# Optimization experiments

Hardware: AMD Instinct MI355X
Metric: run time of the kernel (lower is better)

The kernel has to match this reference:

```python
import jax, jax.numpy as jnp
import numpy as np

N, E, B = 50000, 400000, 8
ND, ED, H, L = 32, 16, 128, 3

def setup_inputs() -> dict:
    key = jax.random.key(0)
    ks = jax.random.split(key, 32)
    s = 0.05
    inp = {
        'x': jax.random.normal(ks[0], (N, ND), jnp.float32),
        'edge_attr': jax.random.normal(ks[1], (E, ED), jnp.float32),
        'global_feature': jax.random.normal(ks[2], (B, 1), jnp.float32),
        'edge_index': jax.random.randint(ks[3], (2, E), 0, N, jnp.int64),
        'batch': jnp.sort(jax.random.randint(ks[4], (N,), 0, B, jnp.int64)),
        # embeddings
        'Wn': jax.random.normal(ks[5], (ND, H), jnp.float32) * s,
        'bn': jnp.zeros((H,), jnp.float32),
        'We': jax.random.normal(ks[6], (ED, H), jnp.float32) * s,
        'be': jnp.zeros((H,), jnp.float32),
        'Wg': jax.random.normal(ks[7], (1, H), jnp.float32) * s,
        'bg': jnp.zeros((H,), jnp.float32),
        # message-passing layers (stacked over L)
        'mW1': jax.random.normal(ks[8], (L, 3 * H, H), jnp.float32) * s,
        'mb1': jnp.zeros((L, H), jnp.float32),
        'mW2': jax.random.normal(ks[9], (L, H, H), jnp.float32) * s,
        'mb2': jnp.zeros((L, H), jnp.float32),
        'uW1': jax.random.normal(ks[10], (L, 2 * H, H), jnp.float32) * s,
        'ub1': jnp.zeros((L, H), jnp.float32),
        'uW2': jax.random.normal(ks[11], (L, H, H), jnp.float32) * s,
        'ub2': jnp.zeros((L, H), jnp.float32),
        # readout MLP
        'rW1': jax.random.normal(ks[12], (2 * H, H), jnp.float32) * s,
        'rb1': jnp.zeros((H,), jnp.float32),
        'rW2': jax.random.normal(ks[13], (H, H // 2), jnp.float32) * s,
        'rb2': jnp.zeros((H // 2,), jnp.float32),
        'rW3': jax.random.normal(ks[14], (H // 2, 1), jnp.float32) * s,
        'rb3': jnp.zeros((1,), jnp.float32),
    }
    return inp

def reference(x, edge_attr, global_feature, Wn, bn, We, be, Wg, bg,
              mW1, mb1, mW2, mb2, uW1, ub1, uW2, ub2,
              rW1, rb1, rW2, rb2, rW3, rb3, edge_index, batch):
    h = x @ Wn + bn                      # [N,H]
    e = edge_attr @ We + be              # [E,H]
    g = global_feature @ Wg + bg         # [B,H]
    src, dst = edge_index[0], edge_index[1]  # PyG: x_j=source, x_i=target, aggregate at target
    for l in range(L):
        m_in = jnp.concatenate([h[dst], h[src], e], axis=1)            # [E,3H]
        m = jax.nn.relu(m_in @ mW1[l] + mb1[l]) @ mW2[l] + mb2[l]       # [E,H]
        aggr = jax.ops.segment_sum(m, dst, num_segments=N)              # [N,H]
        u_in = jnp.concatenate([h, aggr], axis=1)                       # [N,2H]
        upd = jax.nn.relu(u_in @ uW1[l] + ub1[l]) @ uW2[l] + ub2[l]
        h = h + upd
    counts = jax.ops.segment_sum(jnp.ones((N,), h.dtype), batch, num_segments=B)
    pooled = jax.ops.segment_sum(h, batch, num_segments=B) / jnp.maximum(counts, 1.0)[:, None]
    final = jnp.concatenate([pooled, g], axis=1)                        # [B,2H]
    out = jax.nn.relu(final @ rW1 + rb1)
    out = jax.nn.relu(out @ rW2 + rb2)
    return out @ rW3 + rb3                                              # [B,1]
```

## Files before the change

### kernel.cpp

```cpp
#include <hip/hip_runtime.h>

#define NN 50000
#define NPAD 50048
#define NE 400000
#define NBATCH 8
#define NDIM 32
#define EDIM 16
#define H 128
#define NLAYERS 3
#define CHUNK_ELEMS 4096
#define NODE_CHUNKS 24
#define ZW_CHUNK 8192
#define NSB 196
#define ZEB 128

#define EMB_B 1563
#define DEG_B 1563
#define ZWB (NLAYERS * 8)
#define WEFB NLAYERS
#define WUB (NLAYERS * 257)
#define P1_B (EMB_B + DEG_B + ZWB + WEFB + WUB)
#define K2_B (NSB + NLAYERS + NLAYERS * NODE_CHUNKS)
#define ZDZS_B (NPAD / 64)
#define ZE_B (NE / ZEB)
#define ZZ_B (ZDZS_B + ZE_B)

typedef __attribute__((ext_vector_type(8))) __bf16 bf16x8;
typedef __attribute__((ext_vector_type(16))) float f32x16;
typedef __attribute__((ext_vector_type(8))) short short8;
typedef __attribute__((ext_vector_type(2))) float v2f;

__device__ __forceinline__ void block_sync_lds() {
  asm volatile("s_waitcnt lgkmcnt(0)\ns_barrier" ::: "memory");
}
__device__ __forceinline__ v2f bf2f(unsigned u) {
  v2f r;
  r.x = __uint_as_float(u << 16);
  r.y = __uint_as_float(u & 0xffff0000u);
  return r;
}

__global__ __launch_bounds__(256) void p1_kernel(
    const float* __restrict__ x, const float* __restrict__ Wn,
    const float* __restrict__ bn, __bf16* __restrict__ hb,
    const int* __restrict__ ei, int* __restrict__ deg,
    const float* __restrict__ mW1, __bf16* __restrict__ ZW,
    const float* __restrict__ mb1, const float* __restrict__ We,
    const float* __restrict__ be, float* __restrict__ Wef,
    float* __restrict__ bm, const float* __restrict__ uW1,
    const float* __restrict__ mW2, const float* __restrict__ mb2,
    float* __restrict__ Wu, float* __restrict__ va) {
  __shared__ __align__(16) float smem[NDIM * H + 32 * NDIM];
  int bi = blockIdx.x;
  int tid = threadIdx.x;
  if (bi < EMB_B) {
    float* Ws = smem;
    float* xs = smem + NDIM * H;
    int nbase = bi * 32;
    for (int f = tid; f < NDIM * H; f += 256) Ws[f] = Wn[f];
    for (int f = tid; f < 32 * NDIM; f += 256) {
      int gi = nbase * NDIM + f;
      xs[f] = (gi < NN * NDIM) ? x[gi] : 0.f;
    }
    __syncthreads();
    int j = tid & 127, g = tid >> 7;
    float b = bn[j];
    for (int nn = 0; nn < 16; ++nn) {
      int node = nbase + g * 16 + nn;
      if (node < NN) {
        float acc = b;
#pragma unroll
        for (int k = 0; k < NDIM; ++k)
          acc = fmaf(xs[(g * 16 + nn) * NDIM + k], Ws[k * H + j], acc);
        hb[(size_t)node * H + j] = (__bf16)acc;
      }
    }
  } else if (bi < EMB_B + DEG_B) {
    int e = (bi - EMB_B) * 256 + tid;
    if (e < NE) atomicAdd(&deg[ei[NE + e]], 1);
  } else if (bi < EMB_B + DEG_B + ZWB) {
    int bb = bi - EMB_B - DEG_B;
    int l = bb / 8;
    int c = bb % 8;
    const float* w1 = mW1 + (size_t)l * 384 * H;
    __bf16* dst = ZW + ((size_t)l * 8 + c) * ZW_CHUNK;
    for (int it = 0; it < 32; it += 4) {
      float wv[4];
#pragma unroll
      for (int q = 0; q < 4; ++q) {
        int flat = (it + q) * 256 + tid;
        int j = flat & 7;
        int lane = (flat >> 3) & 63;
        int nt = (flat >> 9) & 7;
        int k = c * 16 + ((lane >> 5) << 3) + j;
        int n = nt * 32 + (lane & 31);
        wv[q] = (n < 128) ? w1[(size_t)k * H + n]
                          : w1[(size_t)(128 + k) * H + (n - 128)];
      }
#pragma unroll
      for (int q = 0; q < 4; ++q) {
        int flat = (it + q) * 256 + tid;
        int hilo = flat >> 12;
        __bf16 hi = (__bf16)wv[q];
        __bf16 lo = (__bf16)(wv[q] - (float)hi);
        dst[flat] = hilo ? lo : hi;
      }
    }
  } else if (bi < EMB_B + DEG_B + ZWB + WEFB) {
    int l = bi - (EMB_B + DEG_B + ZWB);
    float* WeS = smem;
    float* beS = smem + 2048;
    for (int f = tid; f < EDIM * H; f += 256) WeS[f] = We[f];
    if (tid < 128) beS[tid] = be[tid];
    __syncthreads();
    if (tid < 128) {
      int n = tid;
      const float* w1 = mW1 + (size_t)l * 384 * H + (size_t)256 * H + n;
      float acc[EDIM];
#pragma unroll
      for (int i = 0; i < EDIM; ++i) acc[i] = 0.f;
      float accb = 0.f;
      for (int c = 0; c < H; c += 4) {
        float w0 = w1[(size_t)(c + 0) * H];
        float w1v = w1[(size_t)(c + 1) * H];
        float w2 = w1[(size_t)(c + 2) * H];
        float w3 = w1[(size_t)(c + 3) * H];
        accb = fmaf(beS[c + 0], w0, accb);
        accb = fmaf(beS[c + 1], w1v, accb);
        accb = fmaf(beS[c + 2], w2, accb);
        accb = fmaf(beS[c + 3], w3, accb);
#pragma unroll
        for (int i = 0; i < EDIM; ++i) {
          acc[i] = fmaf(WeS[i * H + c + 0], w0, acc[i]);
          acc[i] = fmaf(WeS[i * H + c + 1], w1v, acc[i]);
          acc[i] = fmaf(WeS[i * H + c + 2], w2, acc[i]);
          acc[i] = fmaf(WeS[i * H + c + 3], w3, acc[i]);
        }
      }
#pragma unroll
      for (int i = 0; i < EDIM; ++i)
        Wef[((size_t)l * EDIM + i) * H + n] = acc[i];
      bm[l * H + n] = mb1[l * H + n] + accb;
    }
  } else {
    int bb = bi - (EMB_B + DEG_B + ZWB + WEFB);
    int l = bb / 257;
    int r = bb % 257;
    int j = tid & 127, hf = tid >> 7;
    const float* u1 = uW1 + (size_t)l * 256 * H;
    if (r < 128) {
      if (tid < 128) Wu[((size_t)l * 256 + r) * H + j] = u1[(size_t)r * H + j];
    } else {
      float* rowS = smem;
      float* redS = smem + 128;
      if (tid < 128)
        rowS[tid] = (r < 256) ? mW2[((size_t)l * H + (r - 128)) * H + tid]
                              : mb2[l * H + tid];
      __syncthreads();
      int cb = hf * 64;
      float s0 = 0.f, s1 = 0.f, s2 = 0.f, s3 = 0.f;
      for (int c = 0; c < 64; c += 4) {
        float a0 = u1[(size_t)(128 + cb + c + 0) * H + j];
        float a1 = u1[(size_t)(128 + cb + c + 1) * H + j];
        float a2 = u1[(size_t)(128 + cb + c + 2) * H + j];
        float a3 = u1[(size_t)(128 + cb + c + 3) * H + j];
        s0 = fmaf(rowS[cb + c + 0], a0, s0);
        s1 = fmaf(rowS[cb + c + 1], a1, s1);
        s2 = fmaf(rowS[cb + c + 2], a2, s2);
        s3 = fmaf(rowS[cb + c + 3], a3, s3);
      }
      float s = (s0 + s1) + (s2 + s3);
      if (hf == 1) redS[j] = s;
      __syncthreads();
      if (hf == 0) {
        float tot = s + redS[j];
        if (r < 256) Wu[((size_t)l * 256 + r) * H + j] = tot;
        else va[l * H + j] = tot;
      }
    }
  }
}

__global__ __launch_bounds__(256) void k2_kernel(
    const int* __restrict__ deg, int* __restrict__ bsum,
    const float* __restrict__ Wef, __bf16* __restrict__ WefS,
    const float* __restrict__ Wu, const float* __restrict__ uW2,
    __bf16* __restrict__ WnS) {
  __shared__ int ws[4];
  int bi = blockIdx.x;
  int tid = threadIdx.x;
  if (bi < NSB) {
    int i = bi * 256 + tid;
    int lane = tid & 63, wid = tid >> 6;
    int v = (i < NN) ? deg[i] : 0;
#pragma unroll
    for (int off = 32; off; off >>= 1) v += __shfl_down(v, off);
    if (lane == 0) ws[wid] = v;
    __syncthreads();
    if (tid == 0) bsum[bi] = ws[0] + ws[1] + ws[2] + ws[3];
  } else if (bi < NSB + NLAYERS) {
    int l = bi - NSB;
    int nt = tid >> 6, lane = tid & 63;
    int n = nt * 32 + (lane & 31);
    int half = lane >> 5;
    const float* wl = Wef + (size_t)l * EDIM * H;
    __bf16* dst = WefS + (size_t)l * CHUNK_ELEMS;
#pragma unroll
    for (int j = 0; j < 8; ++j) {
      int k = half * 8 + j;
      float w = wl[(size_t)k * H + n];
      __bf16 hi = (__bf16)w;
      __bf16 lo = (__bf16)(w - (float)hi);
      dst[((0 * 4 + nt) * 64 + lane) * 8 + j] = hi;
      dst[((1 * 4 + nt) * 64 + lane) * 8 + j] = lo;
    }
  } else {
    int idx = bi - NSB - NLAYERS;
    int l = idx / NODE_CHUNKS;
    int c = idx % NODE_CHUNKS;
    int nt = tid >> 6, lane = tid & 63;
    int n = nt * 32 + (lane & 31);
    int half = lane >> 5;
    __bf16* dst = WnS + ((size_t)l * NODE_CHUNKS + c) * CHUNK_ELEMS;
#pragma unroll
    for (int j = 0; j < 8; ++j) {
      float w;
      if (c < 16) {
        int k = c * 16 + half * 8 + j;
        w = Wu[((size_t)l * 256 + k) * H + n];
      } else {
        int k = (c - 16) * 16 + half * 8 + j;
        w = uW2[((size_t)l * H + k) * H + n];
      }
      __bf16 hi = (__bf16)w;
      __bf16 lo = (__bf16)(w - (float)hi);
      dst[((0 * 4 + nt) * 64 + lane) * 8 + j] = hi;
      dst[((1 * 4 + nt) * 64 + lane) * 8 + j] = lo;
    }
  }
}

__global__ __launch_bounds__(256) void scan2_kernel(const int* __restrict__ bsum,
                                                    int* __restrict__ boff) {
  __shared__ int s[256];
  int t = threadIdx.x;
  int v = (t < NSB) ? bsum[t] : 0;
  s[t] = v;
  __syncthreads();
  for (int off = 1; off < 256; off <<= 1) {
    int u = (t >= off) ? s[t - off] : 0;
    __syncthreads();
    s[t] += u;
    __syncthreads();
  }
  if (t < NSB) boff[t] = s[t] - v;
}

__global__ __launch_bounds__(256) void scan3_kernel(const int* __restrict__ deg,
                                                    const int* __restrict__ boff,
                                                    int* __restrict__ cursor) {
  __shared__ int wsum[4], woff[4];
  int i = blockIdx.x * 256 + threadIdx.x;
  int lane = threadIdx.x & 63, wid = threadIdx.x >> 6;
  int orig = (i < NN) ? deg[i] : 0;
  int v = orig;
#pragma unroll
  for (int off = 1; off < 64; off <<= 1) {
    int u = __shfl_up(v, off);
    if (lane >= off) v += u;
  }
  if (lane == 63) wsum[wid] = v;
  __syncthreads();
  if (threadIdx.x == 0) {
    int r = 0;
#pragma unroll
    for (int w = 0; w < 4; ++w) {
      woff[w] = r;
      r += wsum[w];
    }
  }
  __syncthreads();
  if (i < NN) cursor[i] = (v - orig) + woff[wid] + boff[blockIdx.x];
}

__global__ __launch_bounds__(256) void scatter_kernel(
    const int* __restrict__ ei, int* __restrict__ cursor,
    int2* __restrict__ seSrt) {
  int e = blockIdx.x * 256 + threadIdx.x;
  if (e < NE) {
    int d = ei[NE + e];
    int pos = atomicAdd(&cursor[d], 1);
    seSrt[pos] = make_int2(ei[e], e);
  }
}

__global__ __launch_bounds__(256) void gather_ea_kernel(
    const float* __restrict__ ea, const int2* __restrict__ seSrt,
    __bf16* __restrict__ eaSrt) {
  int fl = blockIdx.x * 256 + threadIdx.x;
  if (fl < NE) {
    int e = seSrt[fl].y;
    const float4* ep = (const float4*)(ea + (size_t)e * EDIM);
    __bf16* op = eaSrt + (size_t)fl * EDIM;
#pragma unroll
    for (int q = 0; q < 4; ++q) {
      float4 v = ep[q];
      op[q * 4 + 0] = (__bf16)v.x;
      op[q * 4 + 1] = (__bf16)v.y;
      op[q * 4 + 2] = (__bf16)v.z;
      op[q * 4 + 3] = (__bf16)v.w;
    }
  }
}

__global__ __launch_bounds__(256) void zz_kernel(
    const __bf16* __restrict__ hb, const __bf16* __restrict__ ZW,
    const float* __restrict__ bm, __bf16* __restrict__ z,
    const __bf16* __restrict__ eaSrt, const __bf16* __restrict__ WefS,
    __bf16* __restrict__ zePre) {
  __shared__ __align__(16) __bf16 Bt[2][ZW_CHUNK];
  int bi = blockIdx.x;
  int tid = threadIdx.x;
  int wid = tid >> 6, lane = tid & 63, m = lane & 31, half = lane >> 5;
  if (bi < ZDZS_B) {
    int rg = wid & 1;
    int nh = wid >> 1;
    int nb = bi * 64;
    int row = nb + rg * 32 + m;
    const __bf16* aH = hb + (size_t)row * H + half * 8;
    const short8* gW = (const short8*)ZW;
    short8* sB0 = (short8*)&Bt[0][0];
    short8* sB1 = (short8*)&Bt[1][0];
#pragma unroll
    for (int q = 0; q < 4; ++q) sB0[tid + q * 256] = gW[tid + q * 256];
    short8 p0 = gW[1024 + tid], p1 = gW[1024 + tid + 256];
    short8 p2 = gW[1024 + tid + 512], p3 = gW[1024 + tid + 768];
    f32x16 acc[4];
#pragma unroll
    for (int ntl = 0; ntl < 4; ++ntl)
#pragma unroll
      for (int r = 0; r < 16; ++r) acc[ntl][r] = 0.f;
    bf16x8 a = *(const bf16x8*)aH;
    block_sync_lds();

    for (int s = 0; s < 8; ++s) {
      int buf = s & 1;
      bf16x8 na = a;
      if (s + 1 < 8) na = *(const bf16x8*)(aH + (s + 1) * 16);
      if (s + 1 < 8) {
        short8* sb = buf ? sB0 : sB1;
        sb[tid] = p0;
        sb[tid + 256] = p1;
        sb[tid + 512] = p2;
        sb[tid + 768] = p3;
        if (s + 2 < 8) {
          p0 = gW[(size_t)(s + 2) * 1024 + tid];
          p1 = gW[(size_t)(s + 2) * 1024 + tid + 256];
          p2 = gW[(size_t)(s + 2) * 1024 + tid + 512];
          p3 = gW[(size_t)(s + 2) * 1024 + tid + 768];
        }
      }
      const __bf16* bb = &Bt[buf][0];
#pragma unroll
      for (int ntl = 0; ntl < 4; ++ntl) {
        int nt = nh * 4 + ntl;
        bf16x8 bh = *(const bf16x8*)&bb[((0 * 8 + nt) * 64 + lane) * 8];
        bf16x8 bl = *(const bf16x8*)&bb[((1 * 8 + nt) * 64 + lane) * 8];
        acc[ntl] = __builtin_amdgcn_mfma_f32_32x32x16_bf16(a, bh, acc[ntl], 0, 0, 0);
        acc[ntl] = __builtin_amdgcn_mfma_f32_32x32x16_bf16(a, bl, acc[ntl], 0, 0, 0);
      }
      a = na;
      if (s + 1 < 8) block_sync_lds();
    }

    float bmv[4];
#pragma unroll
    for (int ntl = 0; ntl < 4; ++ntl) {
      int nt = nh * 4 + ntl;
      bmv[ntl] = (nt < 4) ? bm[nt * 32 + m] : 0.f;
    }
#pragma unroll
    for (int ntl = 0; ntl < 4; ++ntl) {
      int nt = nh * 4 + ntl;
#pragma unroll
      for (int r = 0; r < 16; ++r) {
        int rowi = (r & 3) + 8 * (r >> 2) + 4 * half;
        z[(size_t)(nb + rg * 32 + rowi) * 256 + nt * 32 + m] =
            (__bf16)(acc[ntl][r] + bmv[ntl]);
      }
    }
  } else {
    __bf16* Bf = &Bt[0][0];
    ((short8*)Bf)[tid] = ((const short8*)WefS)[tid];
    ((short8*)Bf)[tid + 256] = ((const short8*)WefS)[tid + 256];
    int ebase = (bi - ZDZS_B) * ZEB + wid * 32;
    bf16x8 a = *(const bf16x8*)(eaSrt + (size_t)(ebase + m) * EDIM + half * 8);
    f32x16 acc[4];
#pragma unroll
    for (int nt = 0; nt < 4; ++nt)
#pragma unroll
      for (int r = 0; r < 16; ++r) acc[nt][r] = 0.f;
    block_sync_lds();
#pragma unroll
    for (int nt = 0; nt < 4; ++nt) {
      bf16x8 bh = *(const bf16x8*)&Bf[((0 * 4 + nt) * 64 + lane) * 8];
      bf16x8 bl = *(const bf16x8*)&Bf[((1 * 4 + nt) * 64 + lane) * 8];
      acc[nt] = __builtin_amdgcn_mfma_f32_32x32x16_bf16(a, bh, acc[nt], 0, 0, 0);
      acc[nt] = __builtin_amdgcn_mfma_f32_32x32x16_bf16(a, bl, acc[nt], 0, 0, 0);
    }
#pragma unroll
    for (int nt = 0; nt < 4; ++nt) {
#pragma unroll
      for (int r = 0; r < 16; ++r) {
        int rowi = (r & 3) + 8 * (r >> 2) + 4 * half;
        zePre[(size_t)(ebase + rowi) * H + nt * 32 + m] = (__bf16)acc[nt][r];
      }
    }
  }
}

__global__ __launch_bounds__(256) void node_update_mfma_kernel(
    __bf16* __restrict__ hb, const __bf16* __restrict__ z,
    const int2* __restrict__ seSrt, const int* __restrict__ cend,
    const __bf16* __restrict__ zePre, const int* __restrict__ deg,
    const __bf16* __restrict__ WnS, const float* __restrict__ ub1,
    const float* __restrict__ va, const float* __restrict__ ub2) {
  __shared__ __align__(16) __bf16 Bt[2][CHUNK_ELEMS];
  __shared__ __bf16 hid[2][32][132];
  __shared__ float degS[64];
  int tid = threadIdx.x;
  int nb = blockIdx.x * 64;
  if (tid < 64) degS[tid] = (float)deg[nb + tid];
  int wid = tid >> 6, lane = tid & 63, m = lane & 31, half = lane >> 5;
  __bf16* aggrS = &hid[0][0][0];

  {
    int c0 = lane * 2;
    int lr0 = wid * 16;
    int node0 = nb + lr0;
    int start = node0 ? cend[node0 - 1] : 0;
    for (int k = 0; k < 16; ++k) {
      int node = node0 + k;
      int end = cend[node];
      v2f acc2 = {0.f, 0.f};
      if (start < end) {
        v2f zd = bf2f(*(const unsigned*)(z + (size_t)node * 256 + c0));
        int sArr[4];
#pragma unroll
        for (int p = 0; p < 4; ++p)
          if (start + p < end) sArr[p] = seSrt[start + p].x;
        for (int e0 = start; e0 < end; e0 += 4) {
          unsigned zsb[4], zeb[4];
#pragma unroll
          for (int p = 0; p < 4; ++p) {
            if (e0 + p < end) {
              zsb[p] = *(const unsigned*)(z + (size_t)sArr[p] * 256 + 128 + c0);
              zeb[p] = *(const unsigned*)(zePre + (size_t)(e0 + p) * H + c0);
            }
          }
#pragma unroll
          for (int p = 0; p < 4; ++p)
            if (e0 + 4 + p < end) sArr[p] = seSrt[e0 + 4 + p].x;
#pragma unroll
          for (int p = 0; p < 4; ++p) {
            if (e0 + p < end) {
              v2f t = zd + bf2f(zsb[p]) + bf2f(zeb[p]);
              acc2.x += fmaxf(t.x, 0.f);
              acc2.y += fmaxf(t.y, 0.f);
            }
          }
        }
      }
      union { __bf16 b[2]; unsigned u; } pk;
      pk.b[0] = (__bf16)acc2.x;
      pk.b[1] = (__bf16)acc2.y;
      *(unsigned*)(aggrS + (size_t)(lr0 + k) * 132 + c0) = pk.u;
      start = end;
    }
  }

  int rg = wid & 1;
  int nh = wid >> 1;
  int lr = rg * 32 + m;
  int row = nb + lr;
  const __bf16* aHb = hb + (size_t)row * H + half * 8;
  const short8* gW = (const short8*)WnS;
  short8* sB0 = (short8*)&Bt[0][0];
  short8* sB1 = (short8*)&Bt[1][0];
  sB0[tid] = gW[tid];
  sB0[tid + 256] = gW[tid + 256];
  short8 p0 = gW[512 + tid], p1 = gW[512 + tid + 256];
  float bv1[2], bva[2];
#pragma unroll
  for (int ntl = 0; ntl < 2; ++ntl) {
    int nt = nh * 2 + ntl;
    bv1[ntl] = ub1[nt * 32 + m];
    bva[ntl] = va[nt * 32 + m];
  }
  f32x16 acc[2];
#pragma unroll
  for (int ntl = 0; ntl < 2; ++ntl)
#pragma unroll
    for (int r = 0; r < 16; ++r) acc[ntl][r] = 0.f;
  bf16x8 acur = *(const bf16x8*)aHb;
  block_sync_lds();

  for (int s = 0; s < 16; ++s) {
    int buf = s & 1;
    bf16x8 anext = acur;
    if (s + 1 < 16) {
      int sp = s + 1;
      anext = (sp < 8)
                  ? *(const bf16x8*)(aHb + sp * 16)
                  : *(const bf16x8*)(aggrS + (size_t)lr * 132 +
                                     (sp - 8) * 16 + half * 8);
    }
    {
      short8* sb = buf ? sB0 : sB1;
      sb[tid] = p0;
      sb[tid + 256] = p1;
      if (s + 2 < NODE_CHUNKS) {
        p0 = gW[(size_t)(s + 2) * 512 + tid];
        p1 = gW[(size_t)(s + 2) * 512 + tid + 256];
      }
    }
    const __bf16* bb = &Bt[buf][0];
#pragma unroll
    for (int ntl = 0; ntl < 2; ++ntl) {
      int nt = nh * 2 + ntl;
      bf16x8 bh = *(const bf16x8*)&bb[((0 * 4 + nt) * 64 + lane) * 8];
      bf16x8 bl = *(const bf16x8*)&bb[((1 * 4 + nt) * 64 + lane) * 8];
      acc[ntl] = __builtin_amdgcn_mfma_f32_32x32x16_bf16(acur, bh, acc[ntl], 0, 0, 0);
      acc[ntl] = __builtin_amdgcn_mfma_f32_32x32x16_bf16(acur, bl, acc[ntl], 0, 0, 0);
    }
    acur = anext;
    block_sync_lds();
  }

#pragma unroll
  for (int ntl = 0; ntl < 2; ++ntl) {
    int nt = nh * 2 + ntl;
#pragma unroll
    for (int r = 0; r < 16; ++r) {
      int rowi = (r & 3) + 8 * (r >> 2) + 4 * half;
      float v = acc[ntl][r] + bv1[ntl] + degS[rg * 32 + rowi] * bva[ntl];
      hid[rg][rowi][nt * 32 + m] = (__bf16)fmaxf(v, 0.f);
      acc[ntl][r] = 0.f;
    }
  }
  block_sync_lds();

  for (int s = 16; s < NODE_CHUNKS; ++s) {
    int buf = s & 1;
    if (s + 1 < NODE_CHUNKS) {
      short8* sb = buf ? sB0 : sB1;
      sb[tid] = p0;
      sb[tid + 256] = p1;
      if (s + 2 < NODE_CHUNKS) {
        p0 = gW[(size_t)(s + 2) * 512 + tid];
        p1 = gW[(size_t)(s + 2) * 512 + tid + 256];
      }
    }
    bf16x8 ah = *(const bf16x8*)&hid[rg][m][(s - 16) * 16 + half * 8];
    const __bf16* bb = &Bt[buf][0];
#pragma unroll
    for (int ntl = 0; ntl < 2; ++ntl) {
      int nt = nh * 2 + ntl;
      bf16x8 bh = *(const bf16x8*)&bb[((0 * 4 + nt) * 64 + lane) * 8];
      bf16x8 bl = *(const bf16x8*)&bb[((1 * 4 + nt) * 64 + lane) * 8];
      acc[ntl] = __builtin_amdgcn_mfma_f32_32x32x16_bf16(ah, bh, acc[ntl], 0, 0, 0);
      acc[ntl] = __builtin_amdgcn_mfma_f32_32x32x16_bf16(ah, bl, acc[ntl], 0, 0, 0);
    }
    if (s + 1 < NODE_CHUNKS) block_sync_lds();
  }

#pragma unroll
  for (int ntl = 0; ntl < 2; ++ntl) {
    int nt = nh * 2 + ntl;
    float b2 = ub2[nt * 32 + m];
#pragma unroll
    for (int r = 0; r < 16; ++r) {
      int rowi = (r & 3) + 8 * (r >> 2) + 4 * half;
      size_t idx = (size_t)(nb + rg * 32 + rowi) * H + nt * 32 + m;
      float hv = (float)hb[idx];
      hb[idx] = (__bf16)(hv + acc[ntl][r] + b2);
    }
  }
}

__global__ __launch_bounds__(256) void pool_kernel(
    const __bf16* __restrict__ hb, const int* __restrict__ batch,
    float* __restrict__ pooled, int* __restrict__ counts) {
  __shared__ float pS[NBATCH * H];
  __shared__ int cS[NBATCH];
  int tid = threadIdx.x;
  for (int i = tid; i < NBATCH * H; i += 256) pS[i] = 0.f;
  if (tid < NBATCH) cS[tid] = 0;
  __syncthreads();
  int c = tid & 15;
  int r0 = tid >> 4;
  int nbase = blockIdx.x * 128;
  v2f acc4[4] = {{0.f, 0.f}, {0.f, 0.f}, {0.f, 0.f}, {0.f, 0.f}};
  int cnt = 0;
  int cur = -1;
#pragma unroll
  for (int i = 0; i < 8; ++i) {
    int n = nbase + i * 16 + r0;
    if (n >= NN) break;
    int b = batch[n];
    if (b != cur) {
      if (cur >= 0) {
#pragma unroll
        for (int q = 0; q < 4; ++q) {
          atomicAdd(&pS[cur * H + c * 8 + q * 2], acc4[q].x);
          atomicAdd(&pS[cur * H + c * 8 + q * 2 + 1], acc4[q].y);
          acc4[q].x = 0.f;
          acc4[q].y = 0.f;
        }
        if (c == 0) atomicAdd(&cS[cur], cnt);
        cnt = 0;
      }
      cur = b;
    }
    uint4 v = *(const uint4*)(hb + (size_t)n * H + c * 8);
    acc4[0] += bf2f(v.x);
    acc4[1] += bf2f(v.y);
    acc4[2] += bf2f(v.z);
    acc4[3] += bf2f(v.w);
    cnt++;
  }
  if (cur >= 0) {
#pragma unroll
    for (int q = 0; q < 4; ++q) {
      atomicAdd(&pS[cur * H + c * 8 + q * 2], acc4[q].x);
      atomicAdd(&pS[cur * H + c * 8 + q * 2 + 1], acc4[q].y);
    }
    if (c == 0) atomicAdd(&cS[cur], cnt);
  }
  __syncthreads();
  for (int i = tid; i < NBATCH * H; i += 256) {
    float v = pS[i];
    if (v != 0.f) unsafeAtomicAdd(&pooled[i], v);
  }
  if (tid < NBATCH) {
    int cv = cS[tid];
    if (cv) atomicAdd(&counts[tid], cv);
  }
}

__global__ __launch_bounds__(128) void readout_kernel(
    const float* __restrict__ pooled, const int* __restrict__ counts,
    const float* __restrict__ gf, const float* __restrict__ Wg,
    const float* __restrict__ bg, const float* __restrict__ rW1,
    const float* __restrict__ rb1, const float* __restrict__ rW2,
    const float* __restrict__ rb2, const float* __restrict__ rW3,
    const float* __restrict__ rb3, float* __restrict__ out) {
  __shared__ float fin[256];
  __shared__ float t1[128];
  __shared__ float t2[64];
  int j = threadIdx.x;
  int b = blockIdx.x;
  float cnt = (float)counts[b];
  if (cnt < 1.f) cnt = 1.f;
  fin[j] = pooled[b * H + j] / cnt;
  fin[H + j] = fmaf(gf[b], Wg[j], bg[j]);
  __syncthreads();
  float a = rb1[j];
  for (int k = 0; k < 256; ++k) a = fmaf(fin[k], rW1[k * H + j], a);
  t1[j] = fmaxf(a, 0.f);
  __syncthreads();
  if (j < 64) {
    float a2 = rb2[j];
    for (int k = 0; k < 128; ++k) a2 = fmaf(t1[k], rW2[k * 64 + j], a2);
    t2[j] = fmaxf(a2, 0.f);
  }
  __syncthreads();
  if (j < 64) {
    float p = t2[j] * rW3[j];
#pragma unroll
    for (int off = 32; off; off >>= 1) p += __shfl_down(p, off);
    if (j == 0) out[b] = p + rb3[0];
  }
}

extern "C" void kernel_launch(void* const* d_in, const int* in_sizes, int n_in,
                              void* d_out, int out_size, void* d_ws, size_t ws_size,
                              hipStream_t stream) {
  const float* x   = (const float*)d_in[0];
  const float* ea  = (const float*)d_in[1];
  const float* gf  = (const float*)d_in[2];
  const int*   ei  = (const int*)d_in[3];
  const int*   bat = (const int*)d_in[4];
  const float* Wn  = (const float*)d_in[5];
  const float* bn  = (const float*)d_in[6];
  const float* We  = (const float*)d_in[7];
  const float* be  = (const float*)d_in[8];
  const float* Wg  = (const float*)d_in[9];
  const float* bg  = (const float*)d_in[10];
  const float* mW1 = (const float*)d_in[11];
  const float* mb1 = (const float*)d_in[12];
  const float* mW2 = (const float*)d_in[13];
  const float* mb2 = (const float*)d_in[14];
  const float* uW1 = (const float*)d_in[15];
  const float* ub1 = (const float*)d_in[16];
  const float* uW2 = (const float*)d_in[17];
  const float* ub2 = (const float*)d_in[18];
  const float* rW1 = (const float*)d_in[19];
  const float* rb1 = (const float*)d_in[20];
  const float* rW2 = (const float*)d_in[21];
  const float* rb2 = (const float*)d_in[22];
  const float* rW3 = (const float*)d_in[23];
  const float* rb3 = (const float*)d_in[24];

  char* p = (char*)d_ws;
  __bf16* hb     = (__bf16*)p; p += (size_t)NPAD * H * 2;
  __bf16* z      = (__bf16*)p; p += (size_t)NPAD * 256 * 2;
  __bf16* zePre  = (__bf16*)p; p += (size_t)NE * H * 2;
  __bf16* eaSrt  = (__bf16*)p; p += (size_t)NE * EDIM * 2;
  int2*   seSrt  = (int2*)p;   p += (size_t)NE * 8;
  __bf16* ZW     = (__bf16*)p; p += (size_t)NLAYERS * 8 * ZW_CHUNK * 2;
  __bf16* WnS    = (__bf16*)p; p += (size_t)NLAYERS * NODE_CHUNKS * CHUNK_ELEMS * 2;
  __bf16* WefS   = (__bf16*)p; p += (size_t)NLAYERS * CHUNK_ELEMS * 2;
  float*  Wef    = (float*)p;  p += (size_t)NLAYERS * EDIM * H * 4;
  float*  bm     = (float*)p;  p += (size_t)NLAYERS * H * 4;
  float*  Wu     = (float*)p;  p += (size_t)NLAYERS * 256 * H * 4;
  float*  va     = (float*)p;  p += (size_t)NLAYERS * H * 4;
  int*    deg    = (int*)p;    p += (size_t)NPAD * 4;
  int*    cursor = (int*)p;    p += (size_t)NPAD * 4;
  int*    bsum   = (int*)p;    p += 256 * 4;
  int*    boff   = (int*)p;    p += 256 * 4;
  float*  pooled = (float*)p;  p += (size_t)NBATCH * H * 4;
  int*    counts = (int*)p;    p += 64;

  hipMemsetAsync(deg, 0, (size_t)NPAD * 4, stream);
  hipMemsetAsync(cursor, 0, (size_t)NPAD * 4, stream);
  hipMemsetAsync(pooled, 0, (size_t)NBATCH * H * 4, stream);
  hipMemsetAsync(counts, 0, 64, stream);

  p1_kernel<<<P1_B, 256, 0, stream>>>(x, Wn, bn, hb, ei, deg, mW1, ZW, mb1, We,
                                      be, Wef, bm, uW1, mW2, mb2, Wu, va);
  k2_kernel<<<K2_B, 256, 0, stream>>>(deg, bsum, Wef, WefS, Wu, uW2, WnS);
  scan2_kernel<<<1, 256, 0, stream>>>(bsum, boff);
  scan3_kernel<<<NSB, 256, 0, stream>>>(deg, boff, cursor);
  scatter_kernel<<<(NE + 255) / 256, 256, 0, stream>>>(ei, cursor, seSrt);
  gather_ea_kernel<<<(NE + 255) / 256, 256, 0, stream>>>(ea, seSrt, eaSrt);

  for (int l = 0; l < NLAYERS; ++l) {
    zz_kernel<<<ZZ_B, 256, 0, stream>>>(
        hb, ZW + (size_t)l * 8 * ZW_CHUNK, bm + (size_t)l * H, z,
        eaSrt, WefS + (size_t)l * CHUNK_ELEMS, zePre);
    node_update_mfma_kernel<<<NPAD / 64, 256, 0, stream>>>(
        hb, z, seSrt, cursor, zePre, deg,
        WnS + (size_t)l * NODE_CHUNKS * CHUNK_ELEMS,
        ub1 + (size_t)l * H, va + (size_t)l * H, ub2 + (size_t)l * H);
  }

  pool_kernel<<<NPAD / 128, 256, 0, stream>>>(hb, bat, pooled, counts);
  readout_kernel<<<NBATCH, 128, 0, stream>>>(pooled, counts, gf, Wg, bg, rW1,
                                             rb1, rW2, rb2, rW3, rb3,
                                             (float*)d_out);
}
```

Baseline: 506.8 us.

## Split edge aggregation into separate one-node-per-wave kernel before node update

Moves the per-node edge gather/relu/sum out of the node update MFMA kernel into a new kernel where each wave handles one node, writing aggregates to a global bf16 buffer. The fused version had each wave serially walk 16 nodes before the MFMA phase, so the long, irregular gather sat ahead of the matmul with limited parallelism. The split gives far more independent waves to hide gather latency. In exchange it adds one kernel launch per layer and a global round-trip of the aggregate buffer.

```diff
diff --git a/kernel.cpp b/kernel.cpp
--- a/kernel.cpp
+++ b/kernel.cpp
@@ -419,12 +419,55 @@
   }
 }
 
+__global__ __launch_bounds__(256) void edge_aggr_kernel(
+    const __bf16* __restrict__ z, const int2* __restrict__ seSrt,
+    const int* __restrict__ cend, const __bf16* __restrict__ zePre,
+    __bf16* __restrict__ aggrB) {
+  int node = blockIdx.x * 4 + (threadIdx.x >> 6);
+  int lane = threadIdx.x & 63;
+  int c0 = lane * 2;
+  int end = cend[node];
+  int start = node ? cend[node - 1] : 0;
+  v2f acc = {0.f, 0.f};
+  if (start < end) {
+    v2f zd = bf2f(*(const unsigned*)(z + (size_t)node * 256 + c0));
+    int sArr[4];
+#pragma unroll
+    for (int p = 0; p < 4; ++p)
+      if (start + p < end) sArr[p] = seSrt[start + p].x;
+    for (int e0 = start; e0 < end; e0 += 4) {
+      unsigned zsb[4], zeb[4];
+#pragma unroll
+      for (int p = 0; p < 4; ++p) {
+        if (e0 + p < end) {
+          zsb[p] = *(const unsigned*)(z + (size_t)sArr[p] * 256 + 128 + c0);
+          zeb[p] = *(const unsigned*)(zePre + (size_t)(e0 + p) * H + c0);
+        }
+      }
+#pragma unroll
+      for (int p = 0; p < 4; ++p)
+        if (e0 + 4 + p < end) sArr[p] = seSrt[e0 + 4 + p].x;
+#pragma unroll
+      for (int p = 0; p < 4; ++p) {
+        if (e0 + p < end) {
+          v2f t = zd + bf2f(zsb[p]) + bf2f(zeb[p]);
+          acc.x += fmaxf(t.x, 0.f);
+          acc.y += fmaxf(t.y, 0.f);
+        }
+      }
+    }
+  }
+  union { __bf16 b[2]; unsigned u; } pk;
+  pk.b[0] = (__bf16)acc.x;
+  pk.b[1] = (__bf16)acc.y;
+  *(unsigned*)(aggrB + (size_t)node * H + c0) = pk.u;
+}
+
 __global__ __launch_bounds__(256) void node_update_mfma_kernel(
-    __bf16* __restrict__ hb, const __bf16* __restrict__ z,
-    const int2* __restrict__ seSrt, const int* __restrict__ cend,
-    const __bf16* __restrict__ zePre, const int* __restrict__ deg,
-    const __bf16* __restrict__ WnS, const float* __restrict__ ub1,
-    const float* __restrict__ va, const float* __restrict__ ub2) {
+    __bf16* __restrict__ hb, const __bf16* __restrict__ aggrB,
+    const int* __restrict__ deg, const __bf16* __restrict__ WnS,
+    const float* __restrict__ ub1, const float* __restrict__ va,
+    const float* __restrict__ ub2) {
   __shared__ __align__(16) __bf16 Bt[2][CHUNK_ELEMS];
   __shared__ __bf16 hid[2][32][132];
   __shared__ float degS[64];
@@ -432,58 +475,11 @@
   int nb = blockIdx.x * 64;
   if (tid < 64) degS[tid] = (float)deg[nb + tid];
   int wid = tid >> 6, lane = tid & 63, m = lane & 31, half = lane >> 5;
-  __bf16* aggrS = &hid[0][0][0];
-
-  {
-    int c0 = lane * 2;
-    int lr0 = wid * 16;
-    int node0 = nb + lr0;
-    int start = node0 ? cend[node0 - 1] : 0;
-    for (int k = 0; k < 16; ++k) {
-      int node = node0 + k;
-      int end = cend[node];
-      v2f acc2 = {0.f, 0.f};
-      if (start < end) {
-        v2f zd = bf2f(*(const unsigned*)(z + (size_t)node * 256 + c0));
-        int sArr[4];
-#pragma unroll
-        for (int p = 0; p < 4; ++p)
-          if (start + p < end) sArr[p] = seSrt[start + p].x;
-        for (int e0 = start; e0 < end; e0 += 4) {
-          unsigned zsb[4], zeb[4];
-#pragma unroll
-          for (int p = 0; p < 4; ++p) {
-            if (e0 + p < end) {
-              zsb[p] = *(const unsigned*)(z + (size_t)sArr[p] * 256 + 128 + c0);
-              zeb[p] = *(const unsigned*)(zePre + (size_t)(e0 + p) * H + c0);
-            }
-          }
-#pragma unroll
-          for (int p = 0; p < 4; ++p)
-            if (e0 + 4 + p < end) sArr[p] = seSrt[e0 + 4 + p].x;
-#pragma unroll
-          for (int p = 0; p < 4; ++p) {
-            if (e0 + p < end) {
-              v2f t = zd + bf2f(zsb[p]) + bf2f(zeb[p]);
-              acc2.x += fmaxf(t.x, 0.f);
-              acc2.y += fmaxf(t.y, 0.f);
-            }
-          }
-        }
-      }
-      union { __bf16 b[2]; unsigned u; } pk;
-      pk.b[0] = (__bf16)acc2.x;
-      pk.b[1] = (__bf16)acc2.y;
-      *(unsigned*)(aggrS + (size_t)(lr0 + k) * 132 + c0) = pk.u;
-      start = end;
-    }
-  }
-
   int rg = wid & 1;
   int nh = wid >> 1;
-  int lr = rg * 32 + m;
-  int row = nb + lr;
+  int row = nb + rg * 32 + m;
   const __bf16* aHb = hb + (size_t)row * H + half * 8;
+  const __bf16* aGb = aggrB + (size_t)row * H + half * 8;
   const short8* gW = (const short8*)WnS;
   short8* sB0 = (short8*)&Bt[0][0];
   short8* sB1 = (short8*)&Bt[1][0];
@@ -510,10 +506,8 @@
     bf16x8 anext = acur;
     if (s + 1 < 16) {
       int sp = s + 1;
-      anext = (sp < 8)
-                  ? *(const bf16x8*)(aHb + sp * 16)
-                  : *(const bf16x8*)(aggrS + (size_t)lr * 132 +
-                                     (sp - 8) * 16 + half * 8);
+      anext = (sp < 8) ? *(const bf16x8*)(aHb + sp * 16)
+                       : *(const bf16x8*)(aGb + (sp - 8) * 16);
     }
     {
       short8* sb = buf ? sB0 : sB1;
@@ -714,6 +708,7 @@
 
   char* p = (char*)d_ws;
   __bf16* hb     = (__bf16*)p; p += (size_t)NPAD * H * 2;
+  __bf16* aggrB  = (__bf16*)p; p += (size_t)NPAD * H * 2;
   __bf16* z      = (__bf16*)p; p += (size_t)NPAD * 256 * 2;
   __bf16* zePre  = (__bf16*)p; p += (size_t)NE * H * 2;
   __bf16* eaSrt  = (__bf16*)p; p += (size_t)NE * EDIM * 2;
@@ -749,9 +744,10 @@
     zz_kernel<<<ZZ_B, 256, 0, stream>>>(
         hb, ZW + (size_t)l * 8 * ZW_CHUNK, bm + (size_t)l * H, z,
         eaSrt, WefS + (size_t)l * CHUNK_ELEMS, zePre);
+    edge_aggr_kernel<<<NPAD / 4, 256, 0, stream>>>(
+        z, seSrt, cursor, zePre, aggrB);
     node_update_mfma_kernel<<<NPAD / 64, 256, 0, stream>>>(
-        hb, z, seSrt, cursor, zePre, deg,
-        WnS + (size_t)l * NODE_CHUNKS * CHUNK_ELEMS,
+        hb, aggrB, deg, WnS + (size_t)l * NODE_CHUNKS * CHUNK_ELEMS,
         ub1 + (size_t)l * H, va + (size_t)l * H, ub2 + (size_t)l * H);
   }
 
```

After: 498.6 us. Within noise of the previous version (-1.6%).
